# Performance work log

Measured on AMD Instinct MI355X. Metric: run time of the kernel, lower is better.

The kernel has to match this reference:

```python
import jax, jax.numpy as jnp
import numpy as np

EMBED = 1024  # scale uses channel (= embed_size), faithful to original


def setup_inputs() -> dict:
    key = jax.random.key(0)
    k1, k2, k3, k4 = jax.random.split(key, 4)
    B, S, E, H = 4, 4096, EMBED, 64
    x = jax.random.normal(k1, (B, S, E), dtype=jnp.float32)
    Wk = jax.random.normal(k2, (E, H), dtype=jnp.float32) * (E ** -0.5)
    Wq = jax.random.normal(k3, (E, H), dtype=jnp.float32) * (E ** -0.5)
    Wv = jax.random.normal(k4, (E, H), dtype=jnp.float32) * (E ** -0.5)
    return {"x": x, "Wk": Wk, "Wq": Wq, "Wv": Wv}


def reference(x, Wk, Wq, Wv):
    # x: [B,S,E]; Wk/Wq/Wv: [E,H]
    B, S, E = x.shape
    k = jnp.einsum('bse,eh->bsh', x, Wk)
    q = jnp.einsum('bse,eh->bsh', x, Wq)
    v = jnp.einsum('bse,eh->bsh', x, Wv)
    # NOTE: original scales by channel**-0.5 (embed dim), not head_size
    scores = jnp.einsum('bqh,bkh->bqk', q, k) * (E ** -0.5)
    causal = jnp.tril(jnp.ones((S, S), dtype=bool))
    scores = jnp.where(causal, scores, -jnp.inf)
    attn = jax.nn.softmax(scores, axis=-1)
    # dropout treated as identity (eval mode) for deterministic reference
    out = jnp.einsum('bqk,bkh->bqh', attn, v)
    return out
```

## Files before the change

### kernel.cpp

```cpp
#include <hip/hip_runtime.h>
#include <hip/hip_bf16.h>
#include <math.h>

#define BATCH 4
#define SEQ   4096
#define EMB   1024
#define HD    64
#define SCALE 0.03125f
#define NSTRIPE 4

typedef __attribute__((ext_vector_type(8))) short short8;
typedef __attribute__((ext_vector_type(4))) float f32x4;

__device__ __forceinline__ short8 ld8g(const __hip_bfloat16* p) {
    union { uint4 u; short8 s; } cv;
    cv.u = *(const uint4*)p;
    return cv.s;
}
__device__ __forceinline__ short8 ld8l(const void* p) {
    union { uint4 u; short8 s; } cv;
    cv.u = *(const uint4*)p;
    return cv.s;
}
__device__ __forceinline__ unsigned short bfb(float a) {
    union { __hip_bfloat16 h; unsigned short u; } cv;
    cv.h = __hip_bfloat16(a);
    return cv.u;
}

__device__ __forceinline__ void gld16(const void* g, const void* lds_base) {
    __builtin_amdgcn_global_load_lds(
        (const __attribute__((address_space(1))) void*)(unsigned long long)(uintptr_t)g,
        (__attribute__((address_space(3))) void*)(unsigned)(uintptr_t)lds_base,
        16, 0, 0);
}

__global__ __launch_bounds__(256) void prep_w(
    const float* __restrict__ Wk, const float* __restrict__ Wq,
    const float* __restrict__ Wv, __hip_bfloat16* __restrict__ WT)
{
    __shared__ float ls[64][65];
    const int wsel = blockIdx.x >> 4;
    const int kblk = blockIdx.x & 15;
    const int k0   = kblk * 64;
    const float* W = (wsel == 0) ? Wq : (wsel == 1) ? Wk : Wv;
    const int t = threadIdx.x;
#pragma unroll
    for (int i = 0; i < 4; ++i) {
        const int idx = t + i * 256;
        const int row = idx >> 4;
        const int c4  = idx & 15;
        const float4 v = *(const float4*)(W + (size_t)(k0 + row) * HD + c4 * 4);
        ls[row][c4 * 4 + 0] = v.x; ls[row][c4 * 4 + 1] = v.y;
        ls[row][c4 * 4 + 2] = v.z; ls[row][c4 * 4 + 3] = v.w;
    }
    __syncthreads();
    const int h   = t >> 2;
    const int kk0 = (t & 3) * 16;
#pragma unroll
    for (int i = 0; i < 2; ++i) {
        const int kk = kk0 + i * 8;
        union { unsigned short u[8]; uint4 q; } pk;
#pragma unroll
        for (int j = 0; j < 8; ++j) pk.u[j] = bfb(ls[kk + j][h]);
        *(uint4*)(WT + (size_t)(wsel * 64 + h) * EMB + k0 + kk) = pk.q;
    }
}

__global__ __launch_bounds__(256) void gemm_proj(
    const float* __restrict__ x,
    const __hip_bfloat16* __restrict__ WT,
    __hip_bfloat16* __restrict__ qs,
    __hip_bfloat16* __restrict__ kb,
    __hip_bfloat16* __restrict__ vT)
{
    __shared__ __align__(16) char sm[2][8 * 1040 + 24 * 1040];

    const int tid  = threadIdx.x;
    const int lane = tid & 63;
    const int c    = lane & 15;
    const int quad = lane >> 4;
    const int w    = tid >> 6;
    const int rw   = w & 1;
    const int nh   = w >> 1;
    const int R0   = blockIdx.x * 32;

    const int rrA = lane >> 4;
    const int ciA = (lane & 15) ^ (rrA << 1);
    const int rrB = lane >> 3;
    const int ciB = (lane & 7) ^ rrB;

    const int rA  = rw * 16 + c;
    const int gA  = rA >> 2;
    const int rrr = rA & 3;

    f32x4 acc[6];
#pragma unroll
    for (int f = 0; f < 6; ++f) acc[f] = (f32x4){0.f, 0.f, 0.f, 0.f};

#define STAGE(buf, kk)                                                          \
    do {                                                                        \
        char* sA = sm[buf];                                                     \
        char* sB = sm[buf] + 8 * 1040;                                          \
        _Pragma("unroll")                                                       \
        for (int j = 0; j < 2; ++j) {                                           \
            const int g = w * 2 + j;                                            \
            gld16(x + (size_t)(R0 + g * 4 + rrA) * EMB + (kk) + ciA * 4,        \
                  sA + g * 1040);                                               \
        }                                                                       \
        _Pragma("unroll")                                                       \
        for (int j = 0; j < 6; ++j) {                                           \
            const int gb = w * 6 + j;                                           \
            gld16(WT + (size_t)(gb * 8 + rrB) * EMB + (kk) + ciB * 8,           \
                  sB + gb * 1040);                                              \
        }                                                                       \
    } while (0)

    STAGE(0, 0);
    __syncthreads();

    for (int s = 0; s < 16; ++s) {
        const int cur = s & 1, nxt = cur ^ 1;
        if (s < 15) STAGE(nxt, (s + 1) * 64);

        const char* smA = sm[cur];
        const char* smB = sm[cur] + 8 * 1040;
        const char* paBase = smA + gA * 1040 + rrr * 256;
#pragma unroll
        for (int ks = 0; ks < 2; ++ks) {
            const int ci0 = ks * 8 + quad * 2;
            const int ps0 = ci0 ^ (rrr << 1);
            const char* pa = paBase + ps0 * 16;
            const float4 fa = *(const float4*)pa;
            const float4 fb = *(const float4*)(pa + 16);
            union { unsigned short u[8]; short8 s8; } av;
            av.u[0] = bfb(fa.x); av.u[1] = bfb(fa.y);
            av.u[2] = bfb(fa.z); av.u[3] = bfb(fa.w);
            av.u[4] = bfb(fb.x); av.u[5] = bfb(fb.y);
            av.u[6] = bfb(fb.z); av.u[7] = bfb(fb.w);
#pragma unroll
            for (int f = 0; f < 6; ++f) {
                const int n   = nh * 96 + f * 16 + c;
                const int gB  = n >> 3;
                const int rB  = n & 7;
                const int psb = (ks * 4 + quad) ^ rB;
                const short8 bfrag = ld8l(smB + gB * 1040 + rB * 128 + psb * 16);
                acc[f] = __builtin_amdgcn_mfma_f32_16x16x32_bf16(av.s8, bfrag, acc[f], 0, 0, 0);
            }
        }
        __syncthreads();
    }
#undef STAGE

#pragma unroll
    for (int f = 0; f < 6; ++f) {
#pragma unroll
        for (int r = 0; r < 4; ++r) {
            const int m = R0 + rw * 16 + quad * 4 + r;
            const int n = nh * 96 + f * 16 + c;
            const float val = acc[f][r];
            if (n < 64) {
                qs[(size_t)m * HD + n] = __hip_bfloat16(val * SCALE);
            } else if (n < 128) {
                kb[(size_t)m * HD + (n - 64)] = __hip_bfloat16(val);
            } else {
                const int b  = m >> 12;
                const int sq = m & (SEQ - 1);
                const int sp = (sq & ~63) | ((sq & 15) << 2) | ((sq >> 4) & 3);
                vT[((size_t)b * HD + (n - 128)) * SEQ + sp] = __hip_bfloat16(val);
            }
        }
    }
}

__global__ __launch_bounds__(256) void attn_kernel(
    const __hip_bfloat16* __restrict__ qs,
    const __hip_bfloat16* __restrict__ kmat,
    const __hip_bfloat16* __restrict__ vT,
    float* __restrict__ Opart,
    float* __restrict__ Lpart)
{
    __shared__ __align__(16) char smK[64 * 128];
    __shared__ __align__(16) char smV[64 * 128];
    __shared__ unsigned int Ps[4][16 * 36];

    const int tid  = threadIdx.x;
    const int w    = tid >> 6;
    const int lane = tid & 63;
    const int c    = lane & 15;
    const int quad = lane >> 4;

    const int g      = blockIdx.x;
    const int gen    = g >> 8;
    const int jj     = g & 255;
    const int b      = jj & 3;
    const int r_     = jj >> 2;
    const int t      = (gen & 1) ? r_ : 63 - r_;
    const int stripe = gen;
    const int q0w    = t * 64 + w * 16;

    const __hip_bfloat16* kbb = kmat + (size_t)b * SEQ * HD;
    const __hip_bfloat16* vTb = vT + (size_t)b * HD * SEQ;

    const __hip_bfloat16* qp = qs + ((size_t)b * SEQ + q0w + c) * HD + quad * 8;
    const short8 aq0 = ld8g(qp);
    const short8 aq1 = ld8g(qp + 32);

    const int rr = lane >> 3;
    const int ci = (lane & 7) ^ rr;

    f32x4 o0 = {0.f,0.f,0.f,0.f}, o1 = o0, o2 = o0, o3 = o0;
    f32x4 lp = {0.f,0.f,0.f,0.f};
    const f32x4 z = {0.f,0.f,0.f,0.f};

    for (int T = stripe; T <= t; T += NSTRIPE) {
        const int k0 = T << 6;

#pragma unroll
        for (int j = 0; j < 2; ++j) {
            const int grp = w * 2 + j;
            const int row = grp * 8 + rr;
            gld16(kbb + (size_t)(k0 + row) * HD + ci * 8, smK + grp * 1024);
            gld16(vTb + (size_t)row * SEQ + k0 + ci * 8, smV + grp * 1024);
        }
        __syncthreads();

        f32x4 sf[4];
#pragma unroll
        for (int f = 0; f < 4; ++f) {
            const int kr = f * 16 + c;
            const char* kp = smK + kr * 128;
            const short8 bk0 = ld8l(kp + ((quad    ) ^ (kr & 7)) * 16);
            const short8 bk1 = ld8l(kp + ((quad + 4) ^ (kr & 7)) * 16);
            sf[f] = __builtin_amdgcn_mfma_f32_16x16x32_bf16(aq0, bk0, z, 0, 0, 0);
            sf[f] = __builtin_amdgcn_mfma_f32_16x16x32_bf16(aq1, bk1, sf[f], 0, 0, 0);
        }

        if (T == t) {
#pragma unroll
            for (int f = 0; f < 4; ++f) {
                const int key = k0 + f * 16 + c;
#pragma unroll
                for (int r = 0; r < 4; ++r)
                    if (key > q0w + quad * 4 + r) sf[f][r] = -1e30f;
            }
        }

        float p[4][4];
#pragma unroll
        for (int f = 0; f < 4; ++f)
#pragma unroll
            for (int r = 0; r < 4; ++r)
                p[f][r] = __expf(sf[f][r]);
#pragma unroll
        for (int r = 0; r < 4; ++r) {
            lp[r] += (p[0][r] + p[1][r]) + (p[2][r] + p[3][r]);
            uint2 dd;
            dd.x = (unsigned int)bfb(p[0][r]) | ((unsigned int)bfb(p[1][r]) << 16);
            dd.y = (unsigned int)bfb(p[2][r]) | ((unsigned int)bfb(p[3][r]) << 16);
            *(uint2*)&Ps[w][(quad * 4 + r) * 36 + c * 2] = dd;
        }

        const short8 ap0 = ld8l(&Ps[w][c * 36 + quad * 4]);
        const short8 ap1 = ld8l(&Ps[w][c * 36 + 16 + quad * 4]);

#pragma unroll
        for (int f = 0; f < 4; ++f) {
            const int vr = f * 16 + c;
            const char* vp = smV + vr * 128;
            const short8 bv0 = ld8l(vp + ((quad    ) ^ (vr & 7)) * 16);
            const short8 bv1 = ld8l(vp + ((quad + 4) ^ (vr & 7)) * 16);
            f32x4* po = (f == 0) ? &o0 : (f == 1) ? &o1 : (f == 2) ? &o2 : &o3;
            *po = __builtin_amdgcn_mfma_f32_16x16x32_bf16(ap0, bv0, *po, 0, 0, 0);
            *po = __builtin_amdgcn_mfma_f32_16x16x32_bf16(ap1, bv1, *po, 0, 0, 0);
        }
        __syncthreads();
    }

#pragma unroll
    for (int r = 0; r < 4; ++r) {
        float v = lp[r];
        v += __shfl_xor(v, 1, 64);
        v += __shfl_xor(v, 2, 64);
        v += __shfl_xor(v, 4, 64);
        v += __shfl_xor(v, 8, 64);
        lp[r] = v;
    }

    float* ob = Opart + (size_t)stripe * (BATCH * SEQ * HD)
                      + ((size_t)b * SEQ + q0w) * HD;
#pragma unroll
    for (int r = 0; r < 4; ++r) {
        const int row = quad * 4 + r;
        ob[row * HD +  0 + c] = o0[r];
        ob[row * HD + 16 + c] = o1[r];
        ob[row * HD + 32 + c] = o2[r];
        ob[row * HD + 48 + c] = o3[r];
        if (c == 0)
            Lpart[(size_t)stripe * (BATCH * SEQ) + (size_t)b * SEQ + q0w + row] = lp[r];
    }
}

__global__ __launch_bounds__(256) void normalize_kernel(
    float* __restrict__ out,
    const float* __restrict__ Opart,
    const float* __restrict__ Lpart)
{
    const int idx4 = blockIdx.x * 256 + threadIdx.x;
    const int row  = idx4 >> 4;
    const float4* O4 = (const float4*)Opart;
    float4 s = O4[idx4];
    float  l = Lpart[row];
#pragma unroll
    for (int st = 1; st < NSTRIPE; ++st) {
        const float4 v = O4[(size_t)st * (BATCH * SEQ * HD / 4) + idx4];
        s.x += v.x; s.y += v.y; s.z += v.z; s.w += v.w;
        l += Lpart[(size_t)st * (BATCH * SEQ) + row];
    }
    const float inv = 1.0f / l;
    float4 o; o.x = s.x * inv; o.y = s.y * inv; o.z = s.z * inv; o.w = s.w * inv;
    ((float4*)out)[idx4] = o;
}

extern "C" void kernel_launch(void* const* d_in, const int* in_sizes, int n_in,
                              void* d_out, int out_size, void* d_ws, size_t ws_size,
                              hipStream_t stream)
{
    (void)in_sizes; (void)n_in; (void)out_size; (void)ws_size;
    const float* x  = (const float*)d_in[0];
    const float* Wk = (const float*)d_in[1];
    const float* Wq = (const float*)d_in[2];
    const float* Wv = (const float*)d_in[3];
    float* out = (float*)d_out;

    const size_t BSH = (size_t)BATCH * SEQ * HD;
    __hip_bfloat16* qs = (__hip_bfloat16*)d_ws;
    __hip_bfloat16* kb = qs + BSH;
    __hip_bfloat16* vT = kb + BSH;
    __hip_bfloat16* WT = vT + BSH;
    float* Opart = (float*)(WT + 192 * EMB);
    float* Lpart = Opart + (size_t)NSTRIPE * BSH;

    prep_w<<<48, 256, 0, stream>>>(Wk, Wq, Wv, WT);
    gemm_proj<<<BATCH * SEQ / 32, 256, 0, stream>>>(x, WT, qs, kb, vT);
    attn_kernel<<<NSTRIPE * BATCH * (SEQ / 64), 256, 0, stream>>>(qs, kb, vT, Opart, Lpart);
    normalize_kernel<<<BATCH * SEQ * HD / 4 / 256, 256, 0, stream>>>(out, Opart, Lpart);
}
```

Measured before the change: 144.6 us.

## Split projection GEMM over output halves, single-buffer LDS, reorder attention tile schedule

The projection GEMM now launches twice as many blocks, each computing 96 of the 192 output columns for a 32-row slab, and drops the double-buffered LDS staging in favour of a single buffer with load-then-sync. This raises block count and occupancy for the memory-bound projection, but each x tile is now read by two blocks and global loads no longer overlap with MFMA work. Separately, the attention kernel changes the tile order for stripes 2 and 3 to rotate by 16 so long and short causal tiles are spread more evenly across concurrent blocks.

```diff
diff --git a/kernel.cpp b/kernel.cpp
--- a/kernel.cpp
+++ b/kernel.cpp
@@ -74,7 +74,9 @@
     __hip_bfloat16* __restrict__ kb,
     __hip_bfloat16* __restrict__ vT)
 {
-    __shared__ __align__(16) char sm[2][8 * 1040 + 24 * 1040];
+    __shared__ __align__(16) char sm[8 * 1040 + 12 * 1040];
+    char* smA = sm;
+    char* smB = sm + 8 * 1040;
 
     const int tid  = threadIdx.x;
     const int lane = tid & 63;
@@ -82,8 +84,11 @@
     const int quad = lane >> 4;
     const int w    = tid >> 6;
     const int rw   = w & 1;
-    const int nh   = w >> 1;
-    const int R0   = blockIdx.x * 32;
+    const int nq   = w >> 1;
+    const int mblk = blockIdx.x >> 1;
+    const int nh   = blockIdx.x & 1;
+    const int R0   = mblk * 32;
+    const int n0   = nh * 96;
 
     const int rrA = lane >> 4;
     const int ciA = (lane & 15) ^ (rrA << 1);
@@ -93,39 +98,29 @@
     const int rA  = rw * 16 + c;
     const int gA  = rA >> 2;
     const int rrr = rA & 3;
-
-    f32x4 acc[6];
-#pragma unroll
-    for (int f = 0; f < 6; ++f) acc[f] = (f32x4){0.f, 0.f, 0.f, 0.f};
-
-#define STAGE(buf, kk)                                                          \
-    do {                                                                        \
-        char* sA = sm[buf];                                                     \
-        char* sB = sm[buf] + 8 * 1040;                                          \
-        _Pragma("unroll")                                                       \
-        for (int j = 0; j < 2; ++j) {                                           \
-            const int g = w * 2 + j;                                            \
-            gld16(x + (size_t)(R0 + g * 4 + rrA) * EMB + (kk) + ciA * 4,        \
-                  sA + g * 1040);                                               \
-        }                                                                       \
-        _Pragma("unroll")                                                       \
-        for (int j = 0; j < 6; ++j) {                                           \
-            const int gb = w * 6 + j;                                           \
-            gld16(WT + (size_t)(gb * 8 + rrB) * EMB + (kk) + ciB * 8,           \
-                  sB + gb * 1040);                                              \
-        }                                                                       \
-    } while (0)
-
-    STAGE(0, 0);
-    __syncthreads();
+    const char* paBase = smA + gA * 1040 + rrr * 256;
+
+    f32x4 acc[3];
+#pragma unroll
+    for (int f = 0; f < 3; ++f) acc[f] = (f32x4){0.f, 0.f, 0.f, 0.f};
 
     for (int s = 0; s < 16; ++s) {
-        const int cur = s & 1, nxt = cur ^ 1;
-        if (s < 15) STAGE(nxt, (s + 1) * 64);
-
-        const char* smA = sm[cur];
-        const char* smB = sm[cur] + 8 * 1040;
-        const char* paBase = smA + gA * 1040 + rrr * 256;
+        const int k0 = s * 64;
+
+#pragma unroll
+        for (int j = 0; j < 2; ++j) {
+            const int g = w * 2 + j;
+            gld16(x + (size_t)(R0 + g * 4 + rrA) * EMB + k0 + ciA * 4,
+                  smA + g * 1040);
+        }
+#pragma unroll
+        for (int j = 0; j < 3; ++j) {
+            const int gb = w * 3 + j;
+            gld16(WT + (size_t)(n0 + gb * 8 + rrB) * EMB + k0 + ciB * 8,
+                  smB + gb * 1040);
+        }
+        __syncthreads();
+
 #pragma unroll
         for (int ks = 0; ks < 2; ++ks) {
             const int ci0 = ks * 8 + quad * 2;
@@ -139,10 +134,10 @@
             av.u[4] = bfb(fb.x); av.u[5] = bfb(fb.y);
             av.u[6] = bfb(fb.z); av.u[7] = bfb(fb.w);
 #pragma unroll
-            for (int f = 0; f < 6; ++f) {
-                const int n   = nh * 96 + f * 16 + c;
-                const int gB  = n >> 3;
-                const int rB  = n & 7;
+            for (int f = 0; f < 3; ++f) {
+                const int nl  = nq * 48 + f * 16 + c;
+                const int gB  = nl >> 3;
+                const int rB  = nl & 7;
                 const int psb = (ks * 4 + quad) ^ rB;
                 const short8 bfrag = ld8l(smB + gB * 1040 + rB * 128 + psb * 16);
                 acc[f] = __builtin_amdgcn_mfma_f32_16x16x32_bf16(av.s8, bfrag, acc[f], 0, 0, 0);
@@ -150,14 +145,13 @@
         }
         __syncthreads();
     }
-#undef STAGE
-
-#pragma unroll
-    for (int f = 0; f < 6; ++f) {
+
+#pragma unroll
+    for (int f = 0; f < 3; ++f) {
 #pragma unroll
         for (int r = 0; r < 4; ++r) {
             const int m = R0 + rw * 16 + quad * 4 + r;
-            const int n = nh * 96 + f * 16 + c;
+            const int n = n0 + nq * 48 + f * 16 + c;
             const float val = acc[f][r];
             if (n < 64) {
                 qs[(size_t)m * HD + n] = __hip_bfloat16(val * SCALE);
@@ -190,12 +184,16 @@
     const int c    = lane & 15;
     const int quad = lane >> 4;
 
-    const int g      = blockIdx.x;
-    const int gen    = g >> 8;
-    const int jj     = g & 255;
-    const int b      = jj & 3;
-    const int r_     = jj >> 2;
-    const int t      = (gen & 1) ? r_ : 63 - r_;
+    const int g   = blockIdx.x;
+    const int gen = g >> 8;
+    const int jj  = g & 255;
+    const int b   = jj & 3;
+    const int r_  = jj >> 2;
+    int t;
+    if      (gen == 0) t = 63 - r_;
+    else if (gen == 1) t = r_;
+    else if (gen == 2) t = (r_ + 16) & 63;
+    else               t = 63 - ((r_ + 16) & 63);
     const int stripe = gen;
     const int q0w    = t * 64 + w * 16;
 
@@ -342,7 +340,7 @@
     float* Lpart = Opart + (size_t)NSTRIPE * BSH;
 
     prep_w<<<48, 256, 0, stream>>>(Wk, Wq, Wv, WT);
-    gemm_proj<<<BATCH * SEQ / 32, 256, 0, stream>>>(x, WT, qs, kb, vT);
+    gemm_proj<<<2 * BATCH * SEQ / 32, 256, 0, stream>>>(x, WT, qs, kb, vT);
     attn_kernel<<<NSTRIPE * BATCH * (SEQ / 64), 256, 0, stream>>>(qs, kb, vT, Opart, Lpart);
     normalize_kernel<<<BATCH * SEQ * HD / 4 / 256, 256, 0, stream>>>(out, Opart, Lpart);
 }
```

New measurement: 151.9 us. 5.1% more time.
